# Kernel optimization log

Hardware: AMD Instinct MI355X
Metric: run time of the kernel (lower is better)

## Reference

```python
import jax, jax.numpy as jnp
import numpy as np

B, D, N, K = 4, 1024, 2048, 1024
INIT_STD = 0.05  # keras 'random_normal' initializer default stddev


def setup_inputs() -> dict:
    key = jax.random.key(0)
    kx, kq, kk, kv, ko = jax.random.split(key, 5)
    inputs = jax.random.normal(kx, (B, D, N), dtype=jnp.float32)
    W_Q = jax.random.normal(kq, (K, D), dtype=jnp.float32) * INIT_STD
    W_K = jax.random.normal(kk, (K, D), dtype=jnp.float32) * INIT_STD
    W_V = jax.random.normal(kv, (K, D), dtype=jnp.float32) * INIT_STD
    W_O = jax.random.normal(ko, (K, D), dtype=jnp.float32) * INIT_STD
    return {"inputs": inputs, "W_Q": W_Q, "W_K": W_K, "W_V": W_V, "W_O": W_O}


def reference(inputs, W_Q, W_K, W_V, W_O):
    # inputs: (b, d, n) -- feature-major layout, sequence on the last axis.
    b, d, n = inputs.shape
    # Q/K projections fused into a single bilinear form: (W_Q x_i) . (W_K x_j)
    # logits[b, i, j] = x[:, i]^T W_Q^T W_K x[:, j]
    q = jnp.einsum('kd,bdi->bki', W_Q, inputs)          # (b, k, n)
    kk = jnp.einsum('kd,bdj->bkj', W_K, inputs)         # (b, k, n)
    logits = jnp.einsum('bki,bkj->bij', q, kk)          # (b, n, n)
    # Causal mask D: -inf strictly above the diagonal (query i attends j <= i).
    causal = jnp.tril(jnp.ones((n, n), dtype=bool))
    logits = jnp.where(causal, logits, -jnp.inf)
    A = jax.nn.softmax(logits, axis=-1)                 # (b, n_q, n_k)
    # context[:, :, i] = sum_t x[:, :, t] * A[i, t]
    ctx = jnp.einsum('bet,bit->bei', inputs, A)         # (b, d, n)
    # Residual + fused V/O projection: x + W_O^T W_V x A
    out = inputs + jnp.einsum('kd,ke,bei->bdi', W_O, W_V, ctx)
    return out
```

## Files before the change

kernel.cpp:

```cpp
#include <hip/hip_runtime.h>
#include <hip/hip_bf16.h>
#include <math.h>

#define BB 4
#define DD 1024
#define NN 2048
#define KK 1024
#define NT128 16
#define NTRI 136
#define TRI_ELEMS 16384

typedef __attribute__((ext_vector_type(4))) float f32x4;
typedef __attribute__((ext_vector_type(8))) short bfrag;

typedef __attribute__((address_space(1))) const unsigned int gu32;
typedef __attribute__((address_space(3))) unsigned int lu32;

__device__ __forceinline__ void async16(const void* g, void* l) {
  __builtin_amdgcn_global_load_lds((gu32*)g, (lu32*)l, 16, 0, 0);
}

__device__ __forceinline__ ushort f2b(float f) {
  union { float f; unsigned u; } c; c.f = f;
  unsigned u = c.u + 0x7fffu + ((c.u >> 16) & 1u);
  return (ushort)(u >> 16);
}
__device__ __forceinline__ float b2f(ushort h) {
  union { unsigned u; float f; } c; c.u = ((unsigned)h) << 16;
  return c.f;
}


__global__ __launch_bounds__(256) void prep(
    const float* __restrict__ x,
    const float* __restrict__ WQ, const float* __restrict__ WK,
    const float* __restrict__ WV, const float* __restrict__ WO,
    ushort* __restrict__ xhi, ushort* __restrict__ xTh, ushort* __restrict__ xTl,
    ushort* __restrict__ qh, ushort* __restrict__ ql,
    ushort* __restrict__ kh, ushort* __restrict__ kl_,
    ushort* __restrict__ vh, ushort* __restrict__ oh) {
  const int z = blockIdx.z;
  const int tx = threadIdx.x, ty = threadIdx.y;
  __shared__ float tile[32][33];
  if (z < 4) {
    const int b = z;
    const int n0 = blockIdx.x * 32, d0 = blockIdx.y * 32;
    const float* xb = x + (long)b * DD * NN;
    ushort* xhb = xhi + (long)b * DD * NN;
#pragma unroll
    for (int r = 0; r < 4; ++r) {
      const int dl = ty + r * 8;
      const float v = xb[(long)(d0 + dl) * NN + n0 + tx];
      tile[dl][tx] = v;
      xhb[(long)(d0 + dl) * NN + n0 + tx] = f2b(v);
    }
    __syncthreads();
#pragma unroll
    for (int r = 0; r < 4; ++r) {
      const int nl = ty + r * 8;
      const float v = tile[tx][nl];
      const ushort h = f2b(v);
      const long o = (long)b * NN * DD + (long)(n0 + nl) * DD + d0 + tx;
      xTh[o] = h;
      xTl[o] = f2b(v - b2f(h));
    }
  } else {
    const int w = (z - 4) * 2 + (blockIdx.x >> 5);
    const float* W = (w == 0) ? WQ : (w == 1) ? WK : (w == 2) ? WV : WO;
    ushort* Th = (w == 0) ? qh : (w == 1) ? kh : (w == 2) ? vh : oh;
    ushort* Tl = (w == 0) ? ql : (w == 1) ? kl_ : nullptr;
    const int k0 = (blockIdx.x & 31) * 32, d0 = blockIdx.y * 32;
#pragma unroll
    for (int r = 0; r < 4; ++r) {
      const int kl = ty + r * 8;
      tile[kl][tx] = W[(long)(k0 + kl) * DD + d0 + tx];
    }
    __syncthreads();
#pragma unroll
    for (int r = 0; r < 4; ++r) {
      const int dl = ty + r * 8;
      const float v = tile[tx][dl];
      const ushort h = f2b(v);
      const long o = (long)(d0 + dl) * KK + k0 + tx;
      Th[o] = h;
      if (Tl) Tl[o] = f2b(v - b2f(h));
    }
  }
}

__global__ __launch_bounds__(256) void gemm_w(
    const ushort* __restrict__ qh, const ushort* __restrict__ ql,
    const ushort* __restrict__ kh, const ushort* __restrict__ kl_,
    const ushort* __restrict__ vh, const ushort* __restrict__ oh,
    ushort* __restrict__ mqk_h, ushort* __restrict__ mqk_l,
    ushort* __restrict__ mov_h) {
  extern __shared__ ushort smem[];
  ushort* sAh = smem;
  ushort* sAl = smem + 2048;
  ushort* sBh = smem + 4096;
  ushort* sBl = smem + 6144;

  const int id = blockIdx.x;
  const int half = id >> 8;
  const int t = id & 255;
  const int m0 = (t >> 4) * 64, n0 = (t & 15) * 64;
  const ushort* A_h = half ? oh : qh;
  const ushort* B_h = half ? vh : kh;

  const int tid = threadIdx.x;
  const int lane = tid & 63, wave = tid >> 6;
  const int wm = (wave & 1) * 32, wn = (wave >> 1) * 32;
  const int r16 = lane & 15, quad = lane >> 4;
  const int kc = ((lane & 3) ^ ((lane >> 3) & 3)) * 8;
  const int srow = lane >> 2;

  f32x4 acc[2][2];
#pragma unroll
  for (int i = 0; i < 2; ++i)
#pragma unroll
    for (int j = 0; j < 2; ++j) acc[i][j] = (f32x4){0.f, 0.f, 0.f, 0.f};

  for (int k0 = 0; k0 < KK; k0 += 32) {
    __syncthreads();
    {
      const int row = wave * 16 + srow;
      const long aoff = (long)(m0 + row) * KK + k0 + kc;
      const long boff = (long)(n0 + row) * KK + k0 + kc;
      async16(A_h + aoff, sAh + wave * 512);
      async16(B_h + boff, sBh + wave * 512);
      if (half == 0) {
        async16(ql + aoff, sAl + wave * 512);
        async16(kl_ + boff, sBl + wave * 512);
      }
    }
    __syncthreads();

    const int sw = (r16 >> 1) & 3;
    bfrag ah[2], bh[2], al[2], bl[2];
#pragma unroll
    for (int t2 = 0; t2 < 2; ++t2) {
      ah[t2] = *(const bfrag*)&sAh[(wm + t2 * 16 + r16) * 32 + (quad ^ sw) * 8];
      bh[t2] = *(const bfrag*)&sBh[(wn + t2 * 16 + r16) * 32 + (quad ^ sw) * 8];
      if (half == 0) {
        al[t2] = *(const bfrag*)&sAl[(wm + t2 * 16 + r16) * 32 + (quad ^ sw) * 8];
        bl[t2] = *(const bfrag*)&sBl[(wn + t2 * 16 + r16) * 32 + (quad ^ sw) * 8];
      }
    }
#pragma unroll
    for (int mt = 0; mt < 2; ++mt)
#pragma unroll
      for (int nt = 0; nt < 2; ++nt) {
        acc[mt][nt] = __builtin_amdgcn_mfma_f32_16x16x32_bf16(ah[mt], bh[nt], acc[mt][nt], 0, 0, 0);
        if (half == 0) {
          acc[mt][nt] = __builtin_amdgcn_mfma_f32_16x16x32_bf16(ah[mt], bl[nt], acc[mt][nt], 0, 0, 0);
          acc[mt][nt] = __builtin_amdgcn_mfma_f32_16x16x32_bf16(al[mt], bh[nt], acc[mt][nt], 0, 0, 0);
        }
      }
  }

#pragma unroll
  for (int mt = 0; mt < 2; ++mt)
#pragma unroll
    for (int nt = 0; nt < 2; ++nt)
#pragma unroll
      for (int reg = 0; reg < 4; ++reg) {
        const int ml = wm + mt * 16 + quad * 4 + reg;
        const int nl = wn + nt * 16 + r16;
        const float v = acc[mt][nt][reg];
        const long o = (long)(m0 + ml) * DD + n0 + nl;
        if (half == 0) {
          const ushort h = f2b(v);
          mqk_h[o] = h;
          mqk_l[o] = f2b(v - b2f(h));
        } else {
          mov_h[o] = f2b(v);
        }
      }
}

template <int SPLIT, int TRIA, int STORE, int SWIZ>
__global__ __launch_bounds__(256) void gemm_mfma(
    const ushort* __restrict__ Ah, const ushort* __restrict__ Al,
    const ushort* __restrict__ Bh, const ushort* __restrict__ Bl,
    void* __restrict__ C0, void* __restrict__ C1, const float* __restrict__ Res,
    int K, int lda, int ldb, int ldc,
    long bA, long bB, long bC, long bR) {
  extern __shared__ ushort smem[];
  ushort* sAh = smem;
  ushort* sBh = smem + (SPLIT ? 8192 : 4096);
  ushort* sAl = SPLIT ? smem + 4096 : nullptr;
  ushort* sBl = SPLIT ? smem + 12288 : nullptr;

  int b, m0, n0, tiC = 0;
  if (SWIZ == 2) {
    const int g = (blockIdx.x & 7) * 68 + (blockIdx.x >> 3);
    b = g / NTRI;
    int t = g - b * NTRI;
    int ti = 0;
    while ((ti + 1) * (ti + 2) / 2 <= t) ++ti;
    const int tj = t - ti * (ti + 1) / 2;
    m0 = ti * 128; n0 = tj * 128; tiC = t;
  } else if (SWIZ == 1) {
    const int g = (blockIdx.x & 7) * 64 + (blockIdx.x >> 3);
    const int P = g >> 3;
    b = P >> 4;
    m0 = (P & 15) * 128;
    n0 = (g & 7) * 128;
  } else {
    b = blockIdx.z; m0 = blockIdx.y * 128; n0 = blockIdx.x * 128;
  }
  const int kmax = TRIA ? (m0 + 128) : K;
  int triA0 = 0;
  if (TRIA) { const int ti = m0 >> 7; triA0 = ti * (ti + 1) / 2; }

  const ushort* A_h = Ah + (long)b * bA;
  const ushort* B_h = Bh + (long)b * bB;
  const ushort* A_l = SPLIT ? Al + (long)b * bA : nullptr;
  const ushort* B_l = SPLIT ? Bl + (long)b * bB : nullptr;

  const int tid = threadIdx.x;
  const int lane = tid & 63, wave = tid >> 6;
  const int wm = (wave & 1) * 64, wn = (wave >> 1) * 64;
  const int r16 = lane & 15, quad = lane >> 4;
  const int kc = ((lane & 3) ^ ((lane >> 3) & 3)) * 8;

  f32x4 acc[4][4];
#pragma unroll
  for (int i = 0; i < 4; ++i)
#pragma unroll
    for (int j = 0; j < 4; ++j) acc[i][j] = (f32x4){0.f, 0.f, 0.f, 0.f};

  for (int k0 = 0; k0 < kmax; k0 += 32) {
    __syncthreads();
    {
#pragma unroll
      for (int c = 0; c < 2; ++c) {
        const int seg = wave * 2 + c;
        const int row = seg * 16 + (lane >> 2);
        long aoff;
        if (TRIA)
          aoff = (long)(triA0 + (k0 >> 7)) * TRI_ELEMS + (long)row * 128 + (k0 & 127) + kc;
        else
          aoff = (long)(m0 + row) * lda + k0 + kc;
        const long boff = (long)(n0 + row) * ldb + k0 + kc;
        async16(A_h + aoff, sAh + seg * 512);
        async16(B_h + boff, sBh + seg * 512);
        if (SPLIT) {
          async16(A_l + aoff, sAl + seg * 512);
          async16(B_l + boff, sBl + seg * 512);
        }
      }
    }
    __syncthreads();

    const int sw = (r16 >> 1) & 3;
    bfrag ah[4], bh[4], al[4], bl[4];
#pragma unroll
    for (int t4 = 0; t4 < 4; ++t4) {
      ah[t4] = *(const bfrag*)&sAh[(wm + t4 * 16 + r16) * 32 + (quad ^ sw) * 8];
      bh[t4] = *(const bfrag*)&sBh[(wn + t4 * 16 + r16) * 32 + (quad ^ sw) * 8];
      if (SPLIT) {
        al[t4] = *(const bfrag*)&sAl[(wm + t4 * 16 + r16) * 32 + (quad ^ sw) * 8];
        bl[t4] = *(const bfrag*)&sBl[(wn + t4 * 16 + r16) * 32 + (quad ^ sw) * 8];
      }
    }
#pragma unroll
    for (int mt = 0; mt < 4; ++mt)
#pragma unroll
      for (int nt = 0; nt < 4; ++nt) {
        acc[mt][nt] = __builtin_amdgcn_mfma_f32_16x16x32_bf16(ah[mt], bh[nt], acc[mt][nt], 0, 0, 0);
        if (SPLIT) {
          acc[mt][nt] = __builtin_amdgcn_mfma_f32_16x16x32_bf16(ah[mt], bl[nt], acc[mt][nt], 0, 0, 0);
          acc[mt][nt] = __builtin_amdgcn_mfma_f32_16x16x32_bf16(al[mt], bh[nt], acc[mt][nt], 0, 0, 0);
        }
      }
  }

#pragma unroll
  for (int mt = 0; mt < 4; ++mt)
#pragma unroll
    for (int nt = 0; nt < 4; ++nt)
#pragma unroll
      for (int reg = 0; reg < 4; ++reg) {
        const int ml = wm + mt * 16 + quad * 4 + reg;
        const int nl = wn + nt * 16 + r16;
        const float v = acc[mt][nt][reg];
        if (STORE == 0) {
          ushort* Ch = (ushort*)C0 + (long)b * bC;
          ushort* Cl = (ushort*)C1 + (long)b * bC;
          const long o = (long)(m0 + ml) * ldc + n0 + nl;
          const ushort h = f2b(v);
          Ch[o] = h;
          Cl[o] = f2b(v - b2f(h));
        } else if (STORE == 1) {
          float* C = (float*)C0 + (long)b * bC + (long)tiC * TRI_ELEMS;
          C[ml * 128 + nl] = v;
        } else if (STORE == 2) {
          ushort* C = (ushort*)C0 + (long)b * bC;
          C[(long)(m0 + ml) * ldc + n0 + nl] = f2b(v);
        } else {
          float* C = (float*)C0 + (long)b * bC;
          const float* R = Res + (long)b * bR;
          const long o = (long)(m0 + ml) * ldc + n0 + nl;
          C[o] = R[o] + v;
        }
      }
}

__global__ __launch_bounds__(256) void softmax_tri(
    const float* __restrict__ L, ushort* __restrict__ Aout) {
  const int row = blockIdx.x;
  const int b = row >> 11, i = row & (NN - 1);
  const int ti = i >> 7, ml = i & 127;
  const long base = (long)b * ((long)NTRI * TRI_ELEMS);
  const int trib = ti * (ti + 1) / 2;
  const int len = i + 1;
  const int tot = (ti + 1) * 128;
  const int tid = threadIdx.x;
  __shared__ float red[256];
  float vv[8];
  float m = -INFINITY;
#pragma unroll
  for (int u = 0; u < 8; ++u) {
    const int j = tid + u * 256;
    if (j < len) {
      const float v = L[base + (long)(trib + (j >> 7)) * TRI_ELEMS + ml * 128 + (j & 127)];
      vv[u] = v;
      m = fmaxf(m, v);
    }
  }
  red[tid] = m; __syncthreads();
  for (int s = 128; s; s >>= 1) { if (tid < s) red[tid] = fmaxf(red[tid], red[tid + s]); __syncthreads(); }
  m = red[0]; __syncthreads();
  float sum = 0.f;
#pragma unroll
  for (int u = 0; u < 8; ++u) {
    const int j = tid + u * 256;
    if (j < len) { const float e = __expf(vv[u] - m); vv[u] = e; sum += e; }
  }
  red[tid] = sum; __syncthreads();
  for (int s = 128; s; s >>= 1) { if (tid < s) red[tid] += red[tid + s]; __syncthreads(); }
  const float inv = 1.f / red[0];
#pragma unroll
  for (int u = 0; u < 8; ++u) {
    const int j = tid + u * 256;
    if (j < tot) {
      const ushort o = (j < len) ? f2b(vv[u] * inv) : (ushort)0;
      Aout[base + (long)(trib + (j >> 7)) * TRI_ELEMS + ml * 128 + (j & 127)] = o;
    }
  }
}

extern "C" void kernel_launch(void* const* d_in, const int* in_sizes, int n_in,
                              void* d_out, int out_size, void* d_ws, size_t ws_size,
                              hipStream_t stream) {
  const float* x = (const float*)d_in[0];
  const float* WQ = (const float*)d_in[1];
  const float* WK = (const float*)d_in[2];
  const float* WV = (const float*)d_in[3];
  const float* WO = (const float*)d_in[4];
  float* out = (float*)d_out;

  const long XE = (long)BB * DD * NN;
  const long WE = (long)DD * KK;
  ushort* x_hi = (ushort*)d_ws;
  ushort* xTh = x_hi + XE;
  ushort* xTl = xTh + XE;
  ushort* wqT_h = xTl + XE;
  ushort* wqT_l = wqT_h + WE;
  ushort* wkT_h = wqT_l + WE;
  ushort* wkT_l = wkT_h + WE;
  ushort* wvT_h = wkT_l + WE;
  ushort* woT_h = wvT_h + WE;
  ushort* mqk_h = woT_h + WE;
  ushort* mqk_l = mqk_h + WE;
  ushort* mov_h = mqk_l + WE;
  ushort* tTh = mov_h + WE;
  ushort* tTl = tTh + XE;
  float* logits = (float*)(tTl + XE);
  ushort* A_tri = tTh;
  ushort* ctxT = (ushort*)logits;
  const long TRIB = (long)NTRI * TRI_ELEMS;
  const long XB = XE / BB;

  prep<<<dim3(64, 32, 6), dim3(32, 8), 0, stream>>>(
      x, WQ, WK, WV, WO, x_hi, xTh, xTl,
      wqT_h, wqT_l, wkT_h, wkT_l, wvT_h, woT_h);

  gemm_w<<<dim3(512), 256, 16384, stream>>>(
      wqT_h, wqT_l, wkT_h, wkT_l, wvT_h, woT_h, mqk_h, mqk_l, mov_h);

  gemm_mfma<1, 0, 0, 1><<<dim3(512), 256, 32768, stream>>>(
      xTh, xTl, mqk_h, mqk_l, tTh, tTl, nullptr,
      DD, DD, DD, DD, XB, 0, XB, 0);

  gemm_mfma<1, 0, 1, 2><<<dim3(BB * NTRI), 256, 32768, stream>>>(
      xTh, xTl, tTh, tTl, logits, nullptr, nullptr,
      DD, DD, DD, 0, XB, XB, TRIB, 0);

  softmax_tri<<<dim3(BB * NN), 256, 0, stream>>>(logits, A_tri);

  gemm_mfma<0, 1, 2, 1><<<dim3(512), 256, 16384, stream>>>(
      A_tri, nullptr, x_hi, nullptr, ctxT, nullptr, nullptr,
      NN, 0, NN, DD, TRIB, XB, XB, 0);

  gemm_mfma<0, 0, 3, 0><<<dim3(NN / 128, DD / 128, BB), 256, 16384, stream>>>(
      mov_h, nullptr, ctxT, nullptr, out, nullptr, x,
      DD, DD, DD, NN, 0, XB, XB, XB);
}
```

Baseline: 352.9 us.

## Double K-step to 64 and rebalance block-to-XCD mapping in MFMA GEMMs

The MFMA GEMM now stages a K-slice of 64 per iteration instead of 32. LDS tiles are doubled, the XOR swizzle is widened to 8 chunks, and two MFMA sub-steps run per barrier pair, so barriers and load-issue overhead are halved. A new SWIZ=3 mapping for the triangular ctx GEMM pairs short and long row tiles on each XCD for load balance. The final output GEMM moves to a 1D XCD-aware grid. The cost is larger dynamic LDS per block (64 KB for split GEMMs), which may reduce occupancy.

```diff
diff --git a/kernel.cpp b/kernel.cpp
--- a/kernel.cpp
+++ b/kernel.cpp
@@ -29,7 +29,6 @@
   union { unsigned u; float f; } c; c.u = ((unsigned)h) << 16;
   return c.f;
 }
-
 
 __global__ __launch_bounds__(256) void prep(
     const float* __restrict__ x,
@@ -187,9 +186,9 @@
     long bA, long bB, long bC, long bR) {
   extern __shared__ ushort smem[];
   ushort* sAh = smem;
-  ushort* sBh = smem + (SPLIT ? 8192 : 4096);
-  ushort* sAl = SPLIT ? smem + 4096 : nullptr;
-  ushort* sBl = SPLIT ? smem + 12288 : nullptr;
+  ushort* sBh = smem + (SPLIT ? 16384 : 8192);
+  ushort* sAl = SPLIT ? smem + 8192 : nullptr;
+  ushort* sBl = SPLIT ? smem + 24576 : nullptr;
 
   int b, m0, n0, tiC = 0;
   if (SWIZ == 2) {
@@ -206,8 +205,20 @@
     b = P >> 4;
     m0 = (P & 15) * 128;
     n0 = (g & 7) * 128;
+  } else if (SWIZ == 3) {
+    const int xcd = blockIdx.x & 7;
+    const int idx = blockIdx.x >> 3;
+    const int q = idx >> 3;
+    b = q >> 1;
+    const int mt_ = (q & 1) ? (15 - xcd) : xcd;
+    m0 = mt_ * 128;
+    n0 = (idx & 7) * 128;
   } else {
-    b = blockIdx.z; m0 = blockIdx.y * 128; n0 = blockIdx.x * 128;
+    const int g = (blockIdx.x & 7) * 64 + (blockIdx.x >> 3);
+    const int P = g >> 3;
+    b = P >> 4;
+    n0 = (P & 15) * 128;
+    m0 = (g & 7) * 128;
   }
   const int kmax = TRIA ? (m0 + 128) : K;
   int triA0 = 0;
@@ -222,7 +233,8 @@
   const int lane = tid & 63, wave = tid >> 6;
   const int wm = (wave & 1) * 64, wn = (wave >> 1) * 64;
   const int r16 = lane & 15, quad = lane >> 4;
-  const int kc = ((lane & 3) ^ ((lane >> 3) & 3)) * 8;
+  const int kc = ((lane & 7) ^ (lane >> 3)) * 8;
+  const int lrow = lane >> 3;
 
   f32x4 acc[4][4];
 #pragma unroll
@@ -230,13 +242,13 @@
 #pragma unroll
     for (int j = 0; j < 4; ++j) acc[i][j] = (f32x4){0.f, 0.f, 0.f, 0.f};
 
-  for (int k0 = 0; k0 < kmax; k0 += 32) {
+  for (int k0 = 0; k0 < kmax; k0 += 64) {
     __syncthreads();
     {
 #pragma unroll
-      for (int c = 0; c < 2; ++c) {
-        const int seg = wave * 2 + c;
-        const int row = seg * 16 + (lane >> 2);
+      for (int c = 0; c < 4; ++c) {
+        const int seg = wave * 4 + c;
+        const int row = seg * 8 + lrow;
         long aoff;
         if (TRIA)
           aoff = (long)(triA0 + (k0 >> 7)) * TRI_ELEMS + (long)row * 128 + (k0 & 127) + kc;
@@ -253,27 +265,31 @@
     }
     __syncthreads();
 
-    const int sw = (r16 >> 1) & 3;
-    bfrag ah[4], bh[4], al[4], bl[4];
-#pragma unroll
-    for (int t4 = 0; t4 < 4; ++t4) {
-      ah[t4] = *(const bfrag*)&sAh[(wm + t4 * 16 + r16) * 32 + (quad ^ sw) * 8];
-      bh[t4] = *(const bfrag*)&sBh[(wn + t4 * 16 + r16) * 32 + (quad ^ sw) * 8];
-      if (SPLIT) {
-        al[t4] = *(const bfrag*)&sAl[(wm + t4 * 16 + r16) * 32 + (quad ^ sw) * 8];
-        bl[t4] = *(const bfrag*)&sBl[(wn + t4 * 16 + r16) * 32 + (quad ^ sw) * 8];
-      }
-    }
-#pragma unroll
-    for (int mt = 0; mt < 4; ++mt)
-#pragma unroll
-      for (int nt = 0; nt < 4; ++nt) {
-        acc[mt][nt] = __builtin_amdgcn_mfma_f32_16x16x32_bf16(ah[mt], bh[nt], acc[mt][nt], 0, 0, 0);
+    const int sw = r16 & 7;
+#pragma unroll
+    for (int ksub = 0; ksub < 2; ++ksub) {
+      const int ch = ((ksub * 4 + quad) ^ sw) * 8;
+      bfrag ah[4], bh[4], al[4], bl[4];
+#pragma unroll
+      for (int t4 = 0; t4 < 4; ++t4) {
+        ah[t4] = *(const bfrag*)&sAh[(wm + t4 * 16 + r16) * 64 + ch];
+        bh[t4] = *(const bfrag*)&sBh[(wn + t4 * 16 + r16) * 64 + ch];
         if (SPLIT) {
-          acc[mt][nt] = __builtin_amdgcn_mfma_f32_16x16x32_bf16(ah[mt], bl[nt], acc[mt][nt], 0, 0, 0);
-          acc[mt][nt] = __builtin_amdgcn_mfma_f32_16x16x32_bf16(al[mt], bh[nt], acc[mt][nt], 0, 0, 0);
-        }
-      }
+          al[t4] = *(const bfrag*)&sAl[(wm + t4 * 16 + r16) * 64 + ch];
+          bl[t4] = *(const bfrag*)&sBl[(wn + t4 * 16 + r16) * 64 + ch];
+        }
+      }
+#pragma unroll
+      for (int mt = 0; mt < 4; ++mt)
+#pragma unroll
+        for (int nt = 0; nt < 4; ++nt) {
+          acc[mt][nt] = __builtin_amdgcn_mfma_f32_16x16x32_bf16(ah[mt], bh[nt], acc[mt][nt], 0, 0, 0);
+          if (SPLIT) {
+            acc[mt][nt] = __builtin_amdgcn_mfma_f32_16x16x32_bf16(ah[mt], bl[nt], acc[mt][nt], 0, 0, 0);
+            acc[mt][nt] = __builtin_amdgcn_mfma_f32_16x16x32_bf16(al[mt], bh[nt], acc[mt][nt], 0, 0, 0);
+          }
+        }
+    }
   }
 
 #pragma unroll
@@ -390,21 +406,21 @@
   gemm_w<<<dim3(512), 256, 16384, stream>>>(
       wqT_h, wqT_l, wkT_h, wkT_l, wvT_h, woT_h, mqk_h, mqk_l, mov_h);
 
-  gemm_mfma<1, 0, 0, 1><<<dim3(512), 256, 32768, stream>>>(
+  gemm_mfma<1, 0, 0, 1><<<dim3(512), 256, 65536, stream>>>(
       xTh, xTl, mqk_h, mqk_l, tTh, tTl, nullptr,
       DD, DD, DD, DD, XB, 0, XB, 0);
 
-  gemm_mfma<1, 0, 1, 2><<<dim3(BB * NTRI), 256, 32768, stream>>>(
+  gemm_mfma<1, 0, 1, 2><<<dim3(BB * NTRI), 256, 65536, stream>>>(
       xTh, xTl, tTh, tTl, logits, nullptr, nullptr,
       DD, DD, DD, 0, XB, XB, TRIB, 0);
 
   softmax_tri<<<dim3(BB * NN), 256, 0, stream>>>(logits, A_tri);
 
-  gemm_mfma<0, 1, 2, 1><<<dim3(512), 256, 16384, stream>>>(
+  gemm_mfma<0, 1, 2, 3><<<dim3(512), 256, 32768, stream>>>(
       A_tri, nullptr, x_hi, nullptr, ctxT, nullptr, nullptr,
       NN, 0, NN, DD, TRIB, XB, XB, 0);
 
-  gemm_mfma<0, 0, 3, 0><<<dim3(NN / 128, DD / 128, BB), 256, 16384, stream>>>(
+  gemm_mfma<0, 0, 3, 4><<<dim3(512), 256, 32768, stream>>>(
       mov_h, nullptr, ctxT, nullptr, out, nullptr, x,
       DD, DD, DD, NN, 0, XB, XB, XB);
 }
```

Measured after the change: 337.1 us. -4.5%, faster.
